# Kernel tuning notes

Hardware: AMD Instinct MI355X
Metric: run time of the kernel (lower is better)

The kernel has to match this reference:

```python
import jax, jax.numpy as jnp
import numpy as np

N_EMBD = 1024
N_HEAD = 16
HEAD_DIM = N_EMBD // N_HEAD
BLOCK = 2048
BATCH = 2


def setup_inputs() -> dict:
    key = jax.random.key(0)
    ks = jax.random.split(key, 6)
    s_in = 1.0 / np.sqrt(N_EMBD)
    s_hd = 1.0 / np.sqrt(N_EMBD)  # fan-in of c_proj1 is n_head*head_dim = n_embd
    return {
        "x": jax.random.normal(ks[0], (BATCH, BLOCK, N_EMBD), jnp.float32),
        "wq": jax.random.normal(ks[1], (N_EMBD, N_HEAD, HEAD_DIM), jnp.float32) * s_in,
        "wk": jax.random.normal(ks[2], (N_EMBD, N_HEAD, HEAD_DIM), jnp.float32) * s_in,
        "wv": jax.random.normal(ks[3], (N_EMBD, N_HEAD, HEAD_DIM), jnp.float32) * s_in,
        "wp1": jax.random.normal(ks[4], (N_HEAD, HEAD_DIM, N_EMBD), jnp.float32) * s_hd,
        "wp2": jax.random.normal(ks[5], (N_EMBD, N_EMBD), jnp.float32) * s_in,
    }


def reference(x, wq, wk, wv, wp1, wp2):
    # QKV projections: DenseGeneral(features=(H, D), axis=-1), no bias
    q = jnp.einsum('btc,chd->bthd', x, wq)
    k = jnp.einsum('btc,chd->bthd', x, wk)
    v = jnp.einsum('btc,chd->bthd', x, wv)
    scale = HEAD_DIM ** (-0.5)
    wei = jnp.einsum('bqhd,bkhd->bhqk', q, k) * scale  # [B,H,T,T]
    tril = jnp.tril(jnp.ones((BLOCK, BLOCK), dtype=bool))
    wei = jnp.where(tril, wei, -jnp.inf)
    wei = jax.nn.softmax(wei, axis=-1)
    att = jnp.einsum('bhqk,bkhd->bqhd', wei, v)  # [B,T,H,D]
    # c_proj1: DenseGeneral over (-2,-1) -> contract (H,D)
    y = jnp.einsum('bqhd,hdc->bqc', att, wp1)
    # c_proj2: Dense
    out = jnp.einsum('bqc,ce->bqe', y, wp2)
    return out
```

## Files before the change

### kernel.cpp

```cpp
#include <hip/hip_runtime.h>
#include <hip/hip_bf16.h>
#include <stdint.h>

typedef __bf16 bf16;
typedef __bf16 bf16x4 __attribute__((ext_vector_type(4)));
typedef __bf16 bf16x8 __attribute__((ext_vector_type(8)));
typedef float  f32x4  __attribute__((ext_vector_type(4)));

#define MFMA16(a,b,c) __builtin_amdgcn_mfma_f32_16x16x32_bf16((a),(b),(c),0,0,0)

#define TSEQ 2048
#define NE   1024
#define NE3  3072
#define NH   16
#define HD   64
#define MTOK 4096

#if defined(__has_builtin) && __has_builtin(__builtin_amdgcn_exp2f)
#define EXP2F(x) __builtin_amdgcn_exp2f(x)
#else
__device__ __forceinline__ float exp2_fast(float x) {
  float r; asm("v_exp_f32 %0, %1" : "=v"(r) : "v"(x)); return r;
}
#define EXP2F(x) exp2_fast(x)
#endif

__device__ __forceinline__ void gl_lds16(const bf16* g, bf16* l) {
  __builtin_amdgcn_global_load_lds(
      (const __attribute__((address_space(1))) void*)g,
      (__attribute__((address_space(3))) void*)l,
      16, 0, 0);
}

__global__ __launch_bounds__(256) void k_prep(const float* __restrict__ x,
                                              const float* __restrict__ wq,
                                              const float* __restrict__ wk,
                                              const float* __restrict__ wv,
                                              const float* __restrict__ wp2,
                                              const float* __restrict__ wp1,
                                              bf16* __restrict__ xb,
                                              bf16* __restrict__ W3T,
                                              bf16* __restrict__ Wp2T,
                                              bf16* __restrict__ Wp1b) {
  const int id = blockIdx.x;
  if (id < 4096) {
    const int i = id * 256 + threadIdx.x;
    float4 v = reinterpret_cast<const float4*>(x)[i];
    bf16x4 o = { (bf16)v.x, (bf16)v.y, (bf16)v.z, (bf16)v.w };
    reinterpret_cast<bf16x4*>(xb)[i] = o;
    return;
  }
  __shared__ float tile[64][65];
  const int wid = id - 4096;
  const int z  = wid >> 8;
  const int by = (wid >> 4) & 15, bx = wid & 15;
  const int r0 = by * 64, c0 = bx * 64;
  const int lc = threadIdx.x & 63, lr0 = threadIdx.x >> 6;
  if (z == 4) {
#pragma unroll
    for (int i = 0; i < 16; ++i) {
      int lr = i*4 + lr0;
      Wp1b[(size_t)(r0 + lr)*1024 + c0 + lc] = (bf16)wp1[(size_t)(r0 + lr)*1024 + c0 + lc];
    }
    return;
  }
  const float* in = (z == 0) ? wq : (z == 1) ? wk : (z == 2) ? wv : wp2;
  bf16* out = (z < 3) ? (W3T + (size_t)z * 1024 * 1024) : Wp2T;
#pragma unroll
  for (int i = 0; i < 16; ++i) {
    int lr = i*4 + lr0;
    tile[lr][lc] = in[(size_t)(r0 + lr) * 1024 + (c0 + lc)];
  }
  __syncthreads();
#pragma unroll
  for (int i = 0; i < 16; ++i) {
    int lr = i*4 + lr0;
    out[(size_t)(c0 + lr) * 1024 + (r0 + lc)] = (bf16)tile[lc][lr];
  }
}

template<int BN, typename OutT, bool VTF>
__global__ __launch_bounds__(256) void k_gemm_bt(const bf16* __restrict__ A,
                                                 const bf16* __restrict__ Bt,
                                                 OutT* __restrict__ C,
                                                 bf16* __restrict__ VtOut,
                                                 const int M, const int N, const int K) {
  constexpr int NC = BN / 32;
  __shared__ bf16 As[2][128*32];
  __shared__ bf16 Bs[2][BN*32];
  const int tid  = threadIdx.x;
  const int lane = tid & 63;
  const int wave = tid >> 6;
  const int wr = (wave >> 1) * 64;
  const int wc = (wave & 1) * (BN/2);
  const int l15 = lane & 15;
  const int l4  = lane >> 4;

  const int nwg = gridDim.x * gridDim.y;
  int id = blockIdx.y * gridDim.x + blockIdx.x;
  id = (id & 7) * (nwg >> 3) + (id >> 3);
  const int bm = (id / gridDim.x) * 128;
  const int bn = (id % gridDim.x) * BN;

  const int srow = tid >> 2;
  const int scol = ((tid & 3) ^ ((tid >> 3) & 3)) * 8;
  const bf16* ag = A  + (size_t)(bm + srow) * K + scol;
  const bf16* bg = Bt + (size_t)(bn + srow) * K + scol;
  const int kx = (l4 ^ ((l15 >> 1) & 3)) * 8;

  f32x4 acc[4][NC] = {};

  auto stage = [&](int buf, int k0) {
    bf16* al = As[buf] + tid * 8;
    bf16* bl = Bs[buf] + tid * 8;
    gl_lds16(ag + k0,                   al);
    gl_lds16(ag + k0 + (size_t)64 * K,  al + 64*32);
    gl_lds16(bg + k0,                   bl);
    if (BN == 128) gl_lds16(bg + k0 + (size_t)64 * K, bl + 64*32);
  };

  stage(0, 0);
  __syncthreads();
  int cur = 0;
  for (int k0 = 0; k0 < K; k0 += 32) {
    if (k0 + 32 < K) stage(cur ^ 1, k0 + 32);
    bf16x8 af[4], bfr[NC];
#pragma unroll
    for (int m = 0; m < 4; ++m)
      af[m] = *reinterpret_cast<const bf16x8*>(&As[cur][(wr + m*16 + l15)*32 + kx]);
#pragma unroll
    for (int n = 0; n < NC; ++n)
      bfr[n] = *reinterpret_cast<const bf16x8*>(&Bs[cur][(wc + n*16 + l15)*32 + kx]);
#pragma unroll
    for (int m = 0; m < 4; ++m)
#pragma unroll
      for (int n = 0; n < NC; ++n)
        acc[m][n] = MFMA16(af[m], bfr[n], acc[m][n]);
    __syncthreads();
    cur ^= 1;
  }

  if (VTF && bn >= 2048) {
    const int bB  = bm >> 11;
    const int tb0 = (bm & 2047) + wr + l4*4;
#pragma unroll
    for (int m = 0; m < 4; ++m) {
      const int tb = tb0 + m*16;
#pragma unroll
      for (int n = 0; n < NC; ++n) {
        const int dg = (bn - 2048) + wc + n*16 + l15;
        bf16x4 ov;
#pragma unroll
        for (int r = 0; r < 4; ++r) ov[r] = (bf16)acc[m][n][r];
        *reinterpret_cast<bf16x4*>(
            &VtOut[((size_t)(bB*16 + (dg >> 6))*64 + (dg & 63))*2048 + tb]) = ov;
      }
    }
  } else {
#pragma unroll
    for (int m = 0; m < 4; ++m) {
      const int row = bm + wr + m*16 + l4*4;
#pragma unroll
      for (int n = 0; n < NC; ++n) {
        const int col = bn + wc + n*16 + l15;
#pragma unroll
        for (int r = 0; r < 4; ++r)
          C[(size_t)(row + r) * N + col] = (OutT)acc[m][n][r];
      }
    }
  }
}

__global__ __launch_bounds__(256) void k_gemm_out(const bf16* __restrict__ A,
                                                  const bf16* __restrict__ Bt,
                                                  float* __restrict__ C) {
  constexpr int K = 1024, N = 1024, BN = 64;
  __shared__ bf16 As[2][128*32];
  __shared__ bf16 Bs[2][BN*32];
  const int tid  = threadIdx.x;
  const int lane = tid & 63;
  const int wave = tid >> 6;
  const int wr = (wave >> 1) * 64;
  const int wc = (wave & 1) * 32;
  const int l15 = lane & 15;
  const int l4  = lane >> 4;

  const int nwg = gridDim.x * gridDim.y;
  int id = blockIdx.y * gridDim.x + blockIdx.x;
  id = (id & 7) * (nwg >> 3) + (id >> 3);
  const int bm = (id / gridDim.x) * 128;
  const int bn = (id % gridDim.x) * BN;

  const int srow = tid >> 2;
  const int scol = ((tid & 3) ^ ((tid >> 3) & 3)) * 8;
  const bf16* ag = A  + (size_t)(bm + srow) * K + scol;
  const bf16* bg = Bt + (size_t)(bn + srow) * K + scol;
  const int kx = (l4 ^ ((l15 >> 1) & 3)) * 8;

  f32x4 acc[4][2] = {};

  auto stage = [&](int buf, int k0) {
    bf16* al = As[buf] + tid * 8;
    bf16* bl = Bs[buf] + tid * 8;
    gl_lds16(ag + k0,                  al);
    gl_lds16(ag + k0 + (size_t)64 * K, al + 64*32);
    gl_lds16(bg + k0,                  bl);
  };

  stage(0, 0);
  __syncthreads();
  int cur = 0;
  for (int k0 = 0; k0 < K; k0 += 32) {
    if (k0 + 32 < K) stage(cur ^ 1, k0 + 32);
    bf16x8 af[4], bfr[2];
#pragma unroll
    for (int m = 0; m < 4; ++m)
      af[m] = *reinterpret_cast<const bf16x8*>(&As[cur][(wr + m*16 + l15)*32 + kx]);
#pragma unroll
    for (int n = 0; n < 2; ++n)
      bfr[n] = *reinterpret_cast<const bf16x8*>(&Bs[cur][(wc + n*16 + l15)*32 + kx]);
#pragma unroll
    for (int m = 0; m < 4; ++m)
#pragma unroll
      for (int n = 0; n < 2; ++n)
        acc[m][n] = MFMA16(af[m], bfr[n], acc[m][n]);
    __syncthreads();
    cur ^= 1;
  }

#pragma unroll
  for (int m = 0; m < 4; ++m) {
    const int row = bm + wr + m*16 + l4*4;
#pragma unroll
    for (int n = 0; n < 2; ++n) {
      const int col = bn + wc + n*16 + l15;
#pragma unroll
      for (int r = 0; r < 4; ++r)
        C[(size_t)(row + r) * N + col] = acc[m][n][r];
    }
  }
}

__global__ __launch_bounds__(512) void k_attn(const bf16* __restrict__ QKV,
                                              const bf16* __restrict__ Vt,
                                              bf16* __restrict__ O) {
  __shared__ bf16 Ks[2][2*128*32];
  __shared__ bf16 Vs[2][4*64*32];
  __shared__ bf16 Ps[8][4*16*32];

  const int tid  = threadIdx.x;
  const int lane = tid & 63;
  const int wave = tid >> 6;
  const int l15 = lane & 15;
  const int l4  = lane >> 4;

  const int x  = blockIdx.x;
  const int p  = x >> 5;
  const int bh = x & 31;
  const int b  = bh >> 4, h = bh & 15;

  const bf16* Qb = QKV + (size_t)b*TSEQ*NE3 +        h*HD;
  const bf16* Kb = QKV + (size_t)b*TSEQ*NE3 + 1024 + h*HD;
  const bf16* Vb = Vt  + (size_t)bh*HD*TSEQ;
  bf16* Pw = Ps[wave];

  const float SC = 0.125f * 1.44269504f;
  const int swz = (l4 ^ ((l15 >> 1) & 3)) * 8;
  const int key = (l15 >> 1) & 3;

  const int krow = tid >> 2;
  const int kg   = (tid & 3) ^ ((krow >> 1) & 3);
  const int vd   = (tid >> 2) & 63;
  const int vg   = (tid & 3) ^ ((vd >> 1) & 3);
  const int vp0  = tid >> 8;

  auto stage = [&](int buf, int t) {
#pragma unroll
    for (int kk = 0; kk < 2; ++kk)
      gl_lds16(&Kb[(size_t)(t*128 + krow)*NE3 + kk*32 + kg*8],
               &Ks[buf][kk*4096 + tid*8]);
#pragma unroll
    for (int kk = 0; kk < 2; ++kk) {
      const int ksv = kk*2 + vp0;
      gl_lds16(&Vb[(size_t)vd*TSEQ + t*128 + ksv*32 + vg*8],
               &Vs[buf][kk*4096 + tid*8]);
    }
  };

  stage(0, 0);
  __syncthreads();
  int cur = 0;
  int i = 0;

  for (int ci = 0; ci < 2; ++ci) {
    const int c  = ci ? (15 - p) : p;
    const int qw = c*128 + wave*16;

    bf16x8 qf[2];
#pragma unroll
    for (int ks = 0; ks < 2; ++ks) {
      bf16x8 qv = *reinterpret_cast<const bf16x8*>(
          &Qb[(size_t)(qw + l15)*NE3 + ks*32 + l4*8]);
#pragma unroll
      for (int j = 0; j < 8; ++j) qv[j] = (bf16)((float)qv[j] * SC);
      qf[ks] = qv;
    }

    f32x4 ot[4] = {};
    float m_run = -1e30f;
    float l_part = 0.f;

    for (int t = 0; t <= c; ++t, ++i) {
      if (i + 1 < 17) {
        const int nxt = (i + 1 <= p) ? (i + 1) : (i - p);
        stage(cur ^ 1, nxt);
      }

      f32x4 st[8];
#pragma unroll
      for (int kvf = 0; kvf < 8; ++kvf) {
        st[kvf] = f32x4{0.f, 0.f, 0.f, 0.f};
        const int row = kvf*16 + l15;
#pragma unroll
        for (int ks = 0; ks < 2; ++ks) {
          bf16x8 kf = *reinterpret_cast<const bf16x8*>(&Ks[cur][ks*4096 + row*32 + swz]);
          st[kvf] = MFMA16(kf, qf[ks], st[kvf]);
        }
      }

      if (t == c) {
#pragma unroll
        for (int kvf = 0; kvf < 8; ++kvf)
#pragma unroll
          for (int r = 0; r < 4; ++r)
            if (kvf*16 + l4*4 + r > wave*16 + l15) st[kvf][r] = -1e30f;
      }

      float mx = st[0][0];
#pragma unroll
      for (int kvf = 0; kvf < 8; ++kvf)
#pragma unroll
        for (int r = 0; r < 4; ++r) mx = fmaxf(mx, st[kvf][r]);
      mx = fmaxf(mx, __shfl_xor(mx, 16));
      mx = fmaxf(mx, __shfl_xor(mx, 32));

      if (__any(mx > m_run + 8.f)) {
        const float mnew = fmaxf(m_run, mx);
        const float corr = EXP2F(m_run - mnew);
        l_part *= corr;
#pragma unroll
        for (int n2 = 0; n2 < 4; ++n2) ot[n2] *= corr;
        m_run = mnew;
      }

      float rs = 0.f;
#pragma unroll
      for (int kvf = 0; kvf < 8; ++kvf) {
        bf16x4 pk;
#pragma unroll
        for (int r = 0; r < 4; ++r) {
          const float pv = EXP2F(st[kvf][r] - m_run);
          rs += pv;
          pk[r] = (bf16)pv;
        }
        const int gp = (((kvf & 1)*2 + (l4 >> 1)) ^ key);
        *reinterpret_cast<bf16x4*>(
            &Pw[(kvf>>1)*512 + l15*32 + gp*8 + (l4 & 1)*4]) = pk;
      }
      l_part += rs;

      bf16x8 pa[4];
#pragma unroll
      for (int ksv = 0; ksv < 4; ++ksv)
        pa[ksv] = *reinterpret_cast<const bf16x8*>(&Pw[ksv*512 + l15*32 + swz]);
#pragma unroll
      for (int n2 = 0; n2 < 4; ++n2) {
        const int vrow = n2*16 + l15;
#pragma unroll
        for (int ksv = 0; ksv < 4; ++ksv) {
          bf16x8 vf = *reinterpret_cast<const bf16x8*>(&Vs[cur][ksv*2048 + vrow*32 + swz]);
          ot[n2] = MFMA16(vf, pa[ksv], ot[n2]);
        }
      }

      __syncthreads();
      cur ^= 1;
    }

    float l = l_part;
    l += __shfl_xor(l, 16);
    l += __shfl_xor(l, 32);
    const float rl = 1.f / l;
    const size_t row = (size_t)(b*TSEQ + qw + l15);
#pragma unroll
    for (int n2 = 0; n2 < 4; ++n2) {
      bf16x4 ov;
#pragma unroll
      for (int r = 0; r < 4; ++r) ov[r] = (bf16)(ot[n2][r] * rl);
      *reinterpret_cast<bf16x4*>(&O[row*NE + h*HD + n2*16 + l4*4]) = ov;
    }
  }
}

extern "C" void kernel_launch(void* const* d_in, const int* in_sizes, int n_in,
                              void* d_out, int out_size, void* d_ws, size_t ws_size,
                              hipStream_t stream) {
  const float* x   = (const float*)d_in[0];
  const float* wq  = (const float*)d_in[1];
  const float* wk  = (const float*)d_in[2];
  const float* wv  = (const float*)d_in[3];
  const float* wp1 = (const float*)d_in[4];
  const float* wp2 = (const float*)d_in[5];
  float* out = (float*)d_out;

  char* ws = (char*)d_ws;
  const size_t MB = 1024ull * 1024ull;
  bf16* xb   = (bf16*)(ws + 0*MB);
  bf16* W3T  = (bf16*)(ws + 8*MB);
  bf16* wp1b = (bf16*)(ws + 14*MB);
  bf16* wp2T = (bf16*)(ws + 16*MB);
  bf16* WcT  = (bf16*)(ws + 18*MB);
  bf16* QKVb = (bf16*)(ws + 20*MB);
  bf16* Vtb  = (bf16*)(ws + 44*MB);
  bf16* attb = (bf16*)(ws + 52*MB);

  k_prep<<<5376, 256, 0, stream>>>(x, wq, wk, wv, wp2, wp1, xb, W3T, wp2T, wp1b);

  k_gemm_bt<64, bf16, false><<<dim3(16, 8), 256, 0, stream>>>(
      wp2T, wp1b, WcT, nullptr, 1024, 1024, 1024);

  k_gemm_bt<128, bf16, true><<<dim3(24, 32), 256, 0, stream>>>(
      xb, W3T, QKVb, Vtb, MTOK, NE3, NE);

  k_attn<<<dim3(256), 512, 0, stream>>>(QKVb, Vtb, attb);

  k_gemm_out<<<dim3(16, 32), 256, 0, stream>>>(attb, WcT, out);
}
```

Baseline: 122.4 us.

## Split attention blocks into 64-query chunks with 4 waves and 512 blocks

The attention kernel now uses 256-thread blocks that each handle 64-query chunks instead of 128, launching 512 blocks rather than 256. Causal load balancing pairs chunk p with chunk 31-p, and the KV tile schedule and diagonal mask offset are recomputed for 128-wide key tiles. The goal is to fill more CUs on the MI355X and reduce tail imbalance. In exchange, each block stages a whole K/V tile for half as many query rows, so global-to-LDS traffic per query doubles.

```diff
diff --git a/kernel.cpp b/kernel.cpp
--- a/kernel.cpp
+++ b/kernel.cpp
@@ -241,12 +241,12 @@
   }
 }
 
-__global__ __launch_bounds__(512) void k_attn(const bf16* __restrict__ QKV,
+__global__ __launch_bounds__(256) void k_attn(const bf16* __restrict__ QKV,
                                               const bf16* __restrict__ Vt,
                                               bf16* __restrict__ O) {
   __shared__ bf16 Ks[2][2*128*32];
   __shared__ bf16 Vs[2][4*64*32];
-  __shared__ bf16 Ps[8][4*16*32];
+  __shared__ bf16 Ps[4][4*16*32];
 
   const int tid  = threadIdx.x;
   const int lane = tid & 63;
@@ -268,23 +268,25 @@
   const int swz = (l4 ^ ((l15 >> 1) & 3)) * 8;
   const int key = (l15 >> 1) & 3;
 
-  const int krow = tid >> 2;
-  const int kg   = (tid & 3) ^ ((krow >> 1) & 3);
-  const int vd   = (tid >> 2) & 63;
-  const int vg   = (tid & 3) ^ ((vd >> 1) & 3);
-  const int vp0  = tid >> 8;
+  const int srow = tid >> 2;
+  const int sg   = (tid & 3) ^ ((tid >> 3) & 3);
+
+  const int ph = p >> 1;
+  auto tileOf = [&](int j) { return (j <= ph) ? j : (j - ph - 1); };
 
   auto stage = [&](int buf, int t) {
 #pragma unroll
     for (int kk = 0; kk < 2; ++kk)
-      gl_lds16(&Kb[(size_t)(t*128 + krow)*NE3 + kk*32 + kg*8],
-               &Ks[buf][kk*4096 + tid*8]);
-#pragma unroll
-    for (int kk = 0; kk < 2; ++kk) {
-      const int ksv = kk*2 + vp0;
-      gl_lds16(&Vb[(size_t)vd*TSEQ + t*128 + ksv*32 + vg*8],
-               &Vs[buf][kk*4096 + tid*8]);
-    }
+#pragma unroll
+      for (int rr = 0; rr < 2; ++rr) {
+        const int r = rr*64 + srow;
+        gl_lds16(&Kb[(size_t)(t*128 + r)*NE3 + kk*32 + sg*8],
+                 &Ks[buf][kk*4096 + rr*2048 + tid*8]);
+      }
+#pragma unroll
+    for (int ksv = 0; ksv < 4; ++ksv)
+      gl_lds16(&Vb[(size_t)srow*TSEQ + t*128 + ksv*32 + sg*8],
+               &Vs[buf][ksv*2048 + tid*8]);
   };
 
   stage(0, 0);
@@ -293,8 +295,10 @@
   int i = 0;
 
   for (int ci = 0; ci < 2; ++ci) {
-    const int c  = ci ? (15 - p) : p;
-    const int qw = c*128 + wave*16;
+    const int c  = ci ? (31 - p) : p;
+    const int qw = c*64 + wave*16;
+    const int ntc = (c >> 1) + 1;
+    const int rloc = (c & 1)*64 + wave*16 + l15;
 
     bf16x8 qf[2];
 #pragma unroll
@@ -310,11 +314,8 @@
     float m_run = -1e30f;
     float l_part = 0.f;
 
-    for (int t = 0; t <= c; ++t, ++i) {
-      if (i + 1 < 17) {
-        const int nxt = (i + 1 <= p) ? (i + 1) : (i - p);
-        stage(cur ^ 1, nxt);
-      }
+    for (int t = 0; t < ntc; ++t, ++i) {
+      if (i + 1 < 17) stage(cur ^ 1, tileOf(i + 1));
 
       f32x4 st[8];
 #pragma unroll
@@ -328,12 +329,12 @@
         }
       }
 
-      if (t == c) {
+      if (t == ntc - 1) {
 #pragma unroll
         for (int kvf = 0; kvf < 8; ++kvf)
 #pragma unroll
           for (int r = 0; r < 4; ++r)
-            if (kvf*16 + l4*4 + r > wave*16 + l15) st[kvf][r] = -1e30f;
+            if (kvf*16 + l4*4 + r > rloc) st[kvf][r] = -1e30f;
       }
 
       float mx = st[0][0];
@@ -432,7 +433,7 @@
   k_gemm_bt<128, bf16, true><<<dim3(24, 32), 256, 0, stream>>>(
       xb, W3T, QKVb, Vtb, MTOK, NE3, NE);
 
-  k_attn<<<dim3(256), 512, 0, stream>>>(QKVb, Vtb, attb);
+  k_attn<<<dim3(512), 256, 0, stream>>>(QKVb, Vtb, attb);
 
   k_gemm_out<<<dim3(16, 32), 256, 0, stream>>>(attb, WcT, out);
 }
```

New measurement: 126.8 us. +3.7%, slower.

## Stage 256-key K/V tiles per barrier, processing two 128-key subtiles each

Applied to the files above, without the earlier changes.

The attention kernel now stages 256 keys of K and V per double-buffered step instead of 128. Each staged tile is processed as two 128-key subtiles, and the causal bound skips the second half when it is past the diagonal. This halves the number of __syncthreads barriers and stage calls per query chunk, to amortize synchronization and load latency. In exchange, LDS usage per block doubles, which may lower occupancy, and a partially wasted half-tile load occurs at the diagonal.

```diff
diff --git a/kernel.cpp b/kernel.cpp
--- a/kernel.cpp
+++ b/kernel.cpp
@@ -244,8 +244,8 @@
 __global__ __launch_bounds__(512) void k_attn(const bf16* __restrict__ QKV,
                                               const bf16* __restrict__ Vt,
                                               bf16* __restrict__ O) {
-  __shared__ bf16 Ks[2][2*128*32];
-  __shared__ bf16 Vs[2][4*64*32];
+  __shared__ bf16 Ks[2][2*256*32];
+  __shared__ bf16 Vs[2][8*64*32];
   __shared__ bf16 Ps[8][4*16*32];
 
   const int tid  = threadIdx.x;
@@ -268,33 +268,44 @@
   const int swz = (l4 ^ ((l15 >> 1) & 3)) * 8;
   const int key = (l15 >> 1) & 3;
 
-  const int krow = tid >> 2;
-  const int kg   = (tid & 3) ^ ((krow >> 1) & 3);
-  const int vd   = (tid >> 2) & 63;
-  const int vg   = (tid & 3) ^ ((vd >> 1) & 3);
-  const int vp0  = tid >> 8;
+  const int krw = tid >> 2;
+  const int kg4 = tid & 3;
+  const int vs  = tid & 255;
+  const int vd  = vs >> 2;
+  const int vg4 = vs & 3;
+  const int vph = tid >> 8;
+
+  const int ntc1 = (p + 2) >> 1;
+  auto tileOf = [&](int j) { return (j < ntc1) ? j : (j - ntc1); };
 
   auto stage = [&](int buf, int t) {
 #pragma unroll
     for (int kk = 0; kk < 2; ++kk)
-      gl_lds16(&Kb[(size_t)(t*128 + krow)*NE3 + kk*32 + kg*8],
-               &Ks[buf][kk*4096 + tid*8]);
-#pragma unroll
-    for (int kk = 0; kk < 2; ++kk) {
-      const int ksv = kk*2 + vp0;
-      gl_lds16(&Vb[(size_t)vd*TSEQ + t*128 + ksv*32 + vg*8],
-               &Vs[buf][kk*4096 + tid*8]);
+#pragma unroll
+      for (int rr = 0; rr < 2; ++rr) {
+        const int r  = rr*128 + krw;
+        const int gs = kg4 ^ ((r >> 1) & 3);
+        gl_lds16(&Kb[(size_t)(t*256 + r)*NE3 + kk*32 + gs*8],
+                 &Ks[buf][kk*8192 + rr*4096 + tid*8]);
+      }
+#pragma unroll
+    for (int rv = 0; rv < 4; ++rv) {
+      const int pt = rv*2 + vph;
+      const int gs = vg4 ^ ((vd >> 1) & 3);
+      gl_lds16(&Vb[(size_t)vd*TSEQ + t*256 + pt*32 + gs*8],
+               &Vs[buf][rv*4096 + tid*8]);
     }
   };
 
   stage(0, 0);
   __syncthreads();
   int cur = 0;
-  int i = 0;
+  int it = 0;
 
   for (int ci = 0; ci < 2; ++ci) {
     const int c  = ci ? (15 - p) : p;
     const int qw = c*128 + wave*16;
+    const int ntc = (c + 2) >> 1;
 
     bf16x8 qf[2];
 #pragma unroll
@@ -310,76 +321,81 @@
     float m_run = -1e30f;
     float l_part = 0.f;
 
-    for (int t = 0; t <= c; ++t, ++i) {
-      if (i + 1 < 17) {
-        const int nxt = (i + 1 <= p) ? (i + 1) : (i - p);
-        stage(cur ^ 1, nxt);
-      }
-
-      f32x4 st[8];
-#pragma unroll
-      for (int kvf = 0; kvf < 8; ++kvf) {
-        st[kvf] = f32x4{0.f, 0.f, 0.f, 0.f};
-        const int row = kvf*16 + l15;
-#pragma unroll
-        for (int ks = 0; ks < 2; ++ks) {
-          bf16x8 kf = *reinterpret_cast<const bf16x8*>(&Ks[cur][ks*4096 + row*32 + swz]);
-          st[kvf] = MFMA16(kf, qf[ks], st[kvf]);
-        }
-      }
-
-      if (t == c) {
-#pragma unroll
-        for (int kvf = 0; kvf < 8; ++kvf)
-#pragma unroll
-          for (int r = 0; r < 4; ++r)
-            if (kvf*16 + l4*4 + r > wave*16 + l15) st[kvf][r] = -1e30f;
-      }
-
-      float mx = st[0][0];
-#pragma unroll
-      for (int kvf = 0; kvf < 8; ++kvf)
-#pragma unroll
-        for (int r = 0; r < 4; ++r) mx = fmaxf(mx, st[kvf][r]);
-      mx = fmaxf(mx, __shfl_xor(mx, 16));
-      mx = fmaxf(mx, __shfl_xor(mx, 32));
-
-      if (__any(mx > m_run + 8.f)) {
-        const float mnew = fmaxf(m_run, mx);
-        const float corr = EXP2F(m_run - mnew);
-        l_part *= corr;
-#pragma unroll
-        for (int n2 = 0; n2 < 4; ++n2) ot[n2] *= corr;
-        m_run = mnew;
-      }
-
-      float rs = 0.f;
-#pragma unroll
-      for (int kvf = 0; kvf < 8; ++kvf) {
-        bf16x4 pk;
-#pragma unroll
-        for (int r = 0; r < 4; ++r) {
-          const float pv = EXP2F(st[kvf][r] - m_run);
-          rs += pv;
-          pk[r] = (bf16)pv;
-        }
-        const int gp = (((kvf & 1)*2 + (l4 >> 1)) ^ key);
-        *reinterpret_cast<bf16x4*>(
-            &Pw[(kvf>>1)*512 + l15*32 + gp*8 + (l4 & 1)*4]) = pk;
-      }
-      l_part += rs;
-
-      bf16x8 pa[4];
-#pragma unroll
-      for (int ksv = 0; ksv < 4; ++ksv)
-        pa[ksv] = *reinterpret_cast<const bf16x8*>(&Pw[ksv*512 + l15*32 + swz]);
-#pragma unroll
-      for (int n2 = 0; n2 < 4; ++n2) {
-        const int vrow = n2*16 + l15;
-#pragma unroll
-        for (int ksv = 0; ksv < 4; ++ksv) {
-          bf16x8 vf = *reinterpret_cast<const bf16x8*>(&Vs[cur][ksv*2048 + vrow*32 + swz]);
-          ot[n2] = MFMA16(vf, pa[ksv], ot[n2]);
+    for (int t = 0; t < ntc; ++t, ++it) {
+      if (it + 1 < 9) stage(cur ^ 1, tileOf(it + 1));
+
+#pragma unroll
+      for (int hh = 0; hh < 2; ++hh) {
+        const int sp = t*2 + hh;
+        if (sp <= c) {
+          f32x4 st[8];
+#pragma unroll
+          for (int kvf = 0; kvf < 8; ++kvf) {
+            st[kvf] = f32x4{0.f, 0.f, 0.f, 0.f};
+            const int row = kvf*16 + l15;
+#pragma unroll
+            for (int ks = 0; ks < 2; ++ks) {
+              bf16x8 kf = *reinterpret_cast<const bf16x8*>(
+                  &Ks[cur][ks*8192 + hh*4096 + row*32 + swz]);
+              st[kvf] = MFMA16(kf, qf[ks], st[kvf]);
+            }
+          }
+
+          if (sp == c) {
+#pragma unroll
+            for (int kvf = 0; kvf < 8; ++kvf)
+#pragma unroll
+              for (int r = 0; r < 4; ++r)
+                if (kvf*16 + l4*4 + r > wave*16 + l15) st[kvf][r] = -1e30f;
+          }
+
+          float mx = st[0][0];
+#pragma unroll
+          for (int kvf = 0; kvf < 8; ++kvf)
+#pragma unroll
+            for (int r = 0; r < 4; ++r) mx = fmaxf(mx, st[kvf][r]);
+          mx = fmaxf(mx, __shfl_xor(mx, 16));
+          mx = fmaxf(mx, __shfl_xor(mx, 32));
+
+          if (__any(mx > m_run + 8.f)) {
+            const float mnew = fmaxf(m_run, mx);
+            const float corr = EXP2F(m_run - mnew);
+            l_part *= corr;
+#pragma unroll
+            for (int n2 = 0; n2 < 4; ++n2) ot[n2] *= corr;
+            m_run = mnew;
+          }
+
+          float rs = 0.f;
+#pragma unroll
+          for (int kvf = 0; kvf < 8; ++kvf) {
+            bf16x4 pk;
+#pragma unroll
+            for (int r = 0; r < 4; ++r) {
+              const float pv = EXP2F(st[kvf][r] - m_run);
+              rs += pv;
+              pk[r] = (bf16)pv;
+            }
+            const int gp = (((kvf & 1)*2 + (l4 >> 1)) ^ key);
+            *reinterpret_cast<bf16x4*>(
+                &Pw[(kvf>>1)*512 + l15*32 + gp*8 + (l4 & 1)*4]) = pk;
+          }
+          l_part += rs;
+
+          bf16x8 pa[4];
+#pragma unroll
+          for (int ksv = 0; ksv < 4; ++ksv)
+            pa[ksv] = *reinterpret_cast<const bf16x8*>(&Pw[ksv*512 + l15*32 + swz]);
+#pragma unroll
+          for (int n2 = 0; n2 < 4; ++n2) {
+            const int vrow = n2*16 + l15;
+#pragma unroll
+            for (int ksv = 0; ksv < 4; ++ksv) {
+              bf16x8 vf = *reinterpret_cast<const bf16x8*>(
+                  &Vs[cur][hh*8192 + ksv*2048 + vrow*32 + swz]);
+              ot[n2] = MFMA16(vf, pa[ksv], ot[n2]);
+            }
+          }
         }
       }
 
```

New measurement: 123.8 us. No clear change (+1.2%).
